# Kernel tuning notes

Measured on AMD Instinct MI355X. Metric: run time of the kernel, lower is better.

## Reference

```python
import jax, jax.numpy as jnp
import numpy as np

N, E, C, L, NG = 50000, 600000, 128, 7, 512
EPS = 1e-7


def layer_norm(z, g, b):
    mu = z.mean(-1, keepdims=True)
    var = ((z - mu) ** 2).mean(-1, keepdims=True)
    return (z - mu) * jax.lax.rsqrt(var + 1e-5) * g + b


def setup_inputs() -> dict:
    key = jax.random.key(0)
    ks = jax.random.split(key, 16)
    inp = {
        'x': jax.random.randint(ks[0], (N, 9), 0, 64, dtype=jnp.int32),
        'edge_index': jax.random.randint(ks[1], (2, E), 0, N, dtype=jnp.int32),
        'edge_attr': jax.random.randint(ks[2], (E, 3), 0, 8, dtype=jnp.int32),
        'batch': jnp.sort(jax.random.randint(ks[3], (N,), 0, NG, dtype=jnp.int32)),
        'atom_emb': jax.random.normal(ks[4], (9, 64, C), jnp.float32) * 0.1,
        'bond_emb': jax.random.normal(ks[5], (3, 8, C), jnp.float32) * 0.1,
        'vn_emb': jnp.zeros((1, C), jnp.float32),
        'conv_W1': jax.random.normal(ks[6], (L, C, 2 * C), jnp.float32) / np.sqrt(C),
        'conv_b1': jnp.zeros((L, 2 * C), jnp.float32),
        'conv_g1': jnp.ones((L, 2 * C), jnp.float32),
        'conv_bb1': jnp.zeros((L, 2 * C), jnp.float32),
        'conv_W2': jax.random.normal(ks[7], (L, 2 * C, C), jnp.float32) / np.sqrt(2 * C),
        'conv_b2': jnp.zeros((L, C), jnp.float32),
        'norm_g': jnp.ones((L, C), jnp.float32),
        'norm_b': jnp.zeros((L, C), jnp.float32),
        'vn_W1': jax.random.normal(ks[8], (L - 1, C, C), jnp.float32) / np.sqrt(C),
        'vn_b1': jnp.zeros((L - 1, C), jnp.float32),
        'vn_g': jnp.ones((L - 1, C), jnp.float32),
        'vn_bb': jnp.zeros((L - 1, C), jnp.float32),
        'vn_W2': jax.random.normal(ks[9], (L - 1, C, C), jnp.float32) / np.sqrt(C),
        'vn_b2': jnp.zeros((L - 1, C), jnp.float32),
    }
    return inp


def reference(x, edge_index, edge_attr, batch, atom_emb, bond_emb, vn_emb,
              conv_W1, conv_b1, conv_g1, conv_bb1, conv_W2, conv_b2,
              norm_g, norm_b, vn_W1, vn_b1, vn_g, vn_bb, vn_W2, vn_b2):
    src, dst = edge_index[0], edge_index[1]

    # AtomEncoder: sum of per-feature embeddings -> [N, C]
    h = atom_emb[jnp.arange(9), x].sum(axis=1)
    # BondEncoder (conv_encode_edge=False) -> [E, C]
    edge_emb = bond_emb[jnp.arange(3), edge_attr].sum(axis=1)

    # virtual node embedding (one per graph)
    vn = jnp.broadcast_to(vn_emb[0], (NG, C))
    h = h + vn[batch]

    def gen_conv(l, hx):
        # GENConv: msg = relu(x_j + e) + eps; softmax aggregation (t=1); MLP(x+m)
        msg = jax.nn.relu(hx[src] + edge_emb) + EPS                      # [E, C]
        mx = jax.ops.segment_max(msg, dst, num_segments=N)               # [N, C]
        e = jnp.exp(msg - mx[dst])
        den = jax.ops.segment_sum(e, dst, num_segments=N)
        m = jax.ops.segment_sum(msg * (e / (den[dst] + 1e-16)), dst, num_segments=N)
        z = hx + m
        z = jax.nn.relu(layer_norm(z @ conv_W1[l] + conv_b1[l], conv_g1[l], conv_bb1[l]))
        return z @ conv_W2[l] + conv_b2[l]

    # res+ block: Conv -> [Norm -> ReLU -> (VN update) -> Conv + res]*
    h = gen_conv(0, h)
    for l in range(1, L):
        h2 = jax.nn.relu(layer_norm(h, norm_g[l - 1], norm_b[l - 1]))
        vtmp = jax.ops.segment_sum(h2, batch, num_segments=NG) + vn
        v = jax.nn.relu(layer_norm(vtmp @ vn_W1[l - 1] + vn_b1[l - 1], vn_g[l - 1], vn_bb[l - 1]))
        vn = v @ vn_W2[l - 1] + vn_b2[l - 1]
        h2 = h2 + vn[batch]
        h = gen_conv(l, h2) + h
    h = layer_norm(h, norm_g[L - 1], norm_b[L - 1])

    # global_add_pool -> [NG, C]
    return jax.ops.segment_sum(h, batch, num_segments=NG)
```

## Files before the change

kernel.cpp:

```cpp
#include <hip/hip_runtime.h>
#include <hip/hip_bf16.h>
#include <stdint.h>

#define N_NODES 50000
#define N_EDGES 600000
#define CH 128
#define NLAYERS 7
#define NGRAPHS 512

typedef __hip_bfloat16 bf16;
using bf16x8 = __attribute__((ext_vector_type(8))) __bf16;
using f32x4  = __attribute__((ext_vector_type(4))) float;

static __device__ __forceinline__ float b2f(bf16 v){ return __bfloat162float(v); }

__global__ void k_detect(const uint32_t* __restrict__ g, int* __restrict__ flag){
  if (threadIdx.x == 0 && blockIdx.x == 0) flag[0] = (g[0] == 0x3F803F80u) ? 1 : 0;
}

struct Segs { const void* src[12]; float* dst[12]; int n[12]; };

__global__ void k_cvt_all(const int* __restrict__ flag, Segs S){
  int f = flag[0];
  int seg = blockIdx.y;
  int n = S.n[seg];
  const void* src = S.src[seg];
  float* dst = S.dst[seg];
  for (int i = blockIdx.x*blockDim.x + threadIdx.x; i < n; i += gridDim.x*blockDim.x)
    dst[i] = f ? b2f(((const bf16*)src)[i]) : ((const float*)src)[i];
}

__global__ void k_transpose_all(const int* __restrict__ flag,
    const void* W1, const void* W2, const void* vW1, const void* vW2,
    bf16* W1T, bf16* W2T, bf16* vW1T, bf16* vW2T){
  int f = flag[0];
  const int T0 = NLAYERS*128*256, T1 = NLAYERS*256*128;
  const int T2 = (NLAYERS-1)*128*128, T3 = (NLAYERS-1)*128*128;
  int total = T0+T1+T2+T3;
  for (int i = blockIdx.x*blockDim.x + threadIdx.x; i < total; i += gridDim.x*blockDim.x){
    const void* src; bf16* dst; int idx, R, C;
    if (i < T0){ src=W1; dst=W1T; idx=i; R=128; C=256; }
    else if (i < T0+T1){ src=W2; dst=W2T; idx=i-T0; R=256; C=128; }
    else if (i < T0+T1+T2){ src=vW1; dst=vW1T; idx=i-T0-T1; R=128; C=128; }
    else { src=vW2; dst=vW2T; idx=i-T0-T1-T2; R=128; C=128; }
    int l = idx/(R*C); int rem = idx - l*R*C; int r = rem / C; int c = rem - r*C;
    float v = f ? b2f(((const bf16*)src)[idx]) : ((const float*)src)[idx];
    dst[l*R*C + c*R + r] = __float2bfloat16(v);
  }
}

__global__ void k_bondC(const int* __restrict__ flag, const void* __restrict__ bond,
                        float* __restrict__ bondC){
  int f = flag[0];
  int i = blockIdx.x*blockDim.x + threadIdx.x;
  if (i >= 512*128) return;
  int idx = i >> 7, c = i & 127;
  int a0 = idx & 7, a1 = (idx>>3) & 7, a2 = (idx>>6) & 7;
  auto g = [&](int e)->float{ return f ? b2f(((const bf16*)bond)[e]) : ((const float*)bond)[e]; };
  bondC[i] = g((0*8+a0)*128 + c) + g((1*8+a1)*128 + c) + g((2*8+a2)*128 + c);
}

__global__ void k_zero_i32(int* p, int n){
  for (int i = blockIdx.x*blockDim.x + threadIdx.x; i < n; i += gridDim.x*blockDim.x) p[i] = 0;
}

__global__ void k_hist(const int* __restrict__ keys, int* __restrict__ counts, int n){
  for (int i = blockIdx.x*blockDim.x + threadIdx.x; i < n; i += gridDim.x*blockDim.x)
    atomicAdd(&counts[keys[i]], 1);
}

__global__ __launch_bounds__(256) void k_scanA(const int* __restrict__ in, int* __restrict__ out,
                                               int* __restrict__ bsums, int n){
  __shared__ int lds[256];
  int t = threadIdx.x;
  int base = blockIdx.x * 1024;
  int v[4]; int s = 0;
  #pragma unroll
  for (int i=0;i<4;i++){ int idx = base + t*4 + i; int x = (idx<n)? in[idx] : 0; v[i]=x; s+=x; }
  lds[t] = s; __syncthreads();
  for (int off=1; off<256; off<<=1){
    int x = (t>=off)? lds[t-off] : 0;
    __syncthreads();
    lds[t] += x;
    __syncthreads();
  }
  int p = lds[t] - s;
  #pragma unroll
  for (int i=0;i<4;i++){ int idx = base + t*4 + i; if (idx<n) out[idx] = p; p += v[i]; }
  if (t==255) bsums[blockIdx.x] = lds[255];
}

__global__ __launch_bounds__(256) void k_scanB(int* bsums, int nblk){
  __shared__ int lds[256];
  int t = threadIdx.x;
  int v = (t<nblk)? bsums[t] : 0;
  lds[t] = v; __syncthreads();
  for (int off=1; off<256; off<<=1){
    int x = (t>=off)? lds[t-off] : 0;
    __syncthreads();
    lds[t] += x;
    __syncthreads();
  }
  if (t<nblk) bsums[t] = lds[t] - v;
}

__global__ void k_scanC(int* out, const int* bsums, int n){
  for (int i = blockIdx.x*blockDim.x + threadIdx.x; i < n; i += gridDim.x*blockDim.x)
    out[i] += bsums[i >> 10];
}

__global__ void k_scatter(const int* __restrict__ ei, const int* __restrict__ ea,
                          const int* __restrict__ row_ptr, int* __restrict__ fill,
                          uint32_t* __restrict__ csr){
  for (int e = blockIdx.x*blockDim.x + threadIdx.x; e < N_EDGES; e += gridDim.x*blockDim.x){
    int src = ei[e];
    int dst = ei[N_EDGES + e];
    int pos = row_ptr[dst] + atomicAdd(&fill[dst], 1);
    uint32_t a0 = (uint32_t)ea[e*3+0], a1 = (uint32_t)ea[e*3+1], a2 = (uint32_t)ea[e*3+2];
    csr[pos] = (uint32_t)src | ((a0 | (a1<<3) | (a2<<6)) << 16);
  }
}

__global__ void k_gptr(const int* __restrict__ batch, int* __restrict__ gptr){
  int i = blockIdx.x*blockDim.x + threadIdx.x;
  if (i >= N_NODES) return;
  int b = batch[i];
  if (i == 0){ for (int g=0; g<=b; ++g) gptr[g] = 0; }
  else { int bp = batch[i-1]; for (int g=bp+1; g<=b; ++g) gptr[g] = i; }
  if (i == N_NODES-1){ for (int g=b+1; g<=NGRAPHS; ++g) gptr[g] = N_NODES; }
}

__global__ __launch_bounds__(128) void k_atom_encode(const int* __restrict__ x,
    const float* __restrict__ atom_emb, const float* __restrict__ vn_emb,
    uint32_t* __restrict__ hxb){
  int n = blockIdx.x; int c = threadIdx.x;
  float s = vn_emb[c];
  #pragma unroll
  for (int f=0; f<9; ++f){
    int xv = x[n*9+f];
    s += atom_emb[(f*64 + xv)*CH + c];
  }
  float o = __shfl_xor(s, 1);
  if ((c & 1) == 0){
    __hip_bfloat162 p; p.x = __float2bfloat16(s); p.y = __float2bfloat16(o);
    hxb[n*64 + (c>>1)] = *reinterpret_cast<uint32_t*>(&p);
  }
}

__global__ void k_vn_init(const float* __restrict__ vn_emb, float* __restrict__ vn){
  for (int i = blockIdx.x*blockDim.x + threadIdx.x; i < NGRAPHS*CH; i += gridDim.x*blockDim.x)
    vn[i] = vn_emb[i & (CH-1)];
}

__global__ __launch_bounds__(64) void k_aggregate(const uint32_t* __restrict__ hxb,
     const uint32_t* __restrict__ csr, const int* __restrict__ row_ptr,
     const float* __restrict__ bondC, uint32_t* __restrict__ z){
  int n = blockIdx.x; int t = threadIdx.x;
  int s0 = row_ptr[n], s1 = row_ptr[n+1];
  float sa=0.f, sb=0.f, wa=0.f, wb=0.f;
  int i = s0;
  for (; i+4 <= s1; i += 4){
    uint32_t u0=csr[i], u1=csr[i+1], u2=csr[i+2], u3=csr[i+3];
    uint32_t h0 = hxb[(size_t)(u0 & 0xFFFFu)*64 + t];
    uint32_t h1 = hxb[(size_t)(u1 & 0xFFFFu)*64 + t];
    uint32_t h2 = hxb[(size_t)(u2 & 0xFFFFu)*64 + t];
    uint32_t h3 = hxb[(size_t)(u3 & 0xFFFFu)*64 + t];
    float2 c0 = *reinterpret_cast<const float2*>(bondC + (size_t)(u0 >> 16)*128 + 2*t);
    float2 c1 = *reinterpret_cast<const float2*>(bondC + (size_t)(u1 >> 16)*128 + 2*t);
    float2 c2 = *reinterpret_cast<const float2*>(bondC + (size_t)(u2 >> 16)*128 + 2*t);
    float2 c3 = *reinterpret_cast<const float2*>(bondC + (size_t)(u3 >> 16)*128 + 2*t);
    #define EDGE(hp, bc) { \
      float va = __uint_as_float(hp << 16) + bc.x; \
      float vb = __uint_as_float(hp & 0xFFFF0000u) + bc.y; \
      va = fmaxf(va, 0.f) + 1e-7f; vb = fmaxf(vb, 0.f) + 1e-7f; \
      float pa = __expf(va - 10.f), pb = __expf(vb - 10.f); \
      sa += pa; wa += pa*va; sb += pb; wb += pb*vb; }
    EDGE(h0, c0) EDGE(h1, c1) EDGE(h2, c2) EDGE(h3, c3)
  }
  for (; i < s1; ++i){
    uint32_t u = csr[i];
    uint32_t hp = hxb[(size_t)(u & 0xFFFFu)*64 + t];
    float2 bc = *reinterpret_cast<const float2*>(bondC + (size_t)(u >> 16)*128 + 2*t);
    EDGE(hp, bc)
    #undef EDGE
  }
  uint32_t own = hxb[(size_t)n*64 + t];
  float za = __uint_as_float(own << 16)         + wa/(sa + 1e-16f);
  float zb = __uint_as_float(own & 0xFFFF0000u) + wb/(sb + 1e-16f);
  __hip_bfloat162 p; p.x = __float2bfloat16(za); p.y = __float2bfloat16(zb);
  z[(size_t)n*64 + t] = *reinterpret_cast<uint32_t*>(&p);
}

template<int K, int N1, int N2>
__global__ __launch_bounds__(512, 2) void k_mlp2(const bf16* __restrict__ A,
    const bf16* __restrict__ W1T, const float* __restrict__ b1,
    const float* __restrict__ g1, const float* __restrict__ bb1,
    const bf16* __restrict__ W2T, const float* __restrict__ b2,
    const float* __restrict__ residual, float* __restrict__ out, int M)
{
  constexpr int KK1 = K/32;
  constexpr int J1  = N1/16/8;
  constexpr int KK2 = N1/32;
  __shared__ float lnp[64][8][2];
  __shared__ float lnv[64][2];
  __shared__ __align__(16) bf16 zt[64*N1];
  const int tid = threadIdx.x;
  const int wid = tid >> 6, lane = tid & 63;
  const int rlo = lane & 15, hi = lane >> 4, khi = hi*8;
  const int row0 = blockIdx.x*64;

  bf16x8 B1[J1][KK1];
  #pragma unroll
  for (int jj=0;jj<J1;++jj){
    int col = (wid*J1 + jj)*16 + rlo;
    #pragma unroll
    for (int kk=0;kk<KK1;++kk)
      B1[jj][kk] = *reinterpret_cast<const bf16x8*>(W1T + (size_t)col*K + kk*32 + khi);
  }
  bf16x8 B2[KK2];
  #pragma unroll
  for (int kk=0;kk<KK2;++kk)
    B2[kk] = *reinterpret_cast<const bf16x8*>(W2T + (size_t)(wid*16 + rlo)*N1 + kk*32 + khi);

  f32x4 acc1[4][J1];
  #pragma unroll
  for (int t=0;t<4;++t)
    #pragma unroll
    for (int jj=0;jj<J1;++jj) acc1[t][jj] = {0.f,0.f,0.f,0.f};
  #pragma unroll
  for (int t=0;t<4;++t){
    int arow = row0 + t*16 + rlo; if (arow >= M) arow = M-1;
    const bf16* ap = A + (size_t)arow*K + khi;
    bf16x8 a[KK1];
    #pragma unroll
    for (int kk=0;kk<KK1;++kk) a[kk] = *reinterpret_cast<const bf16x8*>(ap + kk*32);
    #pragma unroll
    for (int kk=0;kk<KK1;++kk)
      #pragma unroll
      for (int jj=0;jj<J1;++jj)
        acc1[t][jj] = __builtin_amdgcn_mfma_f32_16x16x32_bf16(a[kk], B1[jj][kk], acc1[t][jj], 0,0,0);
  }

  float b1v[J1];
  #pragma unroll
  for (int jj=0;jj<J1;++jj) b1v[jj] = b1[(wid*J1+jj)*16 + rlo];
  float p[4][4], q[4][4];
  #pragma unroll
  for (int t=0;t<4;++t)
    #pragma unroll
    for (int r=0;r<4;++r){ p[t][r]=0.f; q[t][r]=0.f; }
  #pragma unroll
  for (int t=0;t<4;++t)
    #pragma unroll
    for (int jj=0;jj<J1;++jj)
      #pragma unroll
      for (int r=0;r<4;++r){
        float v = acc1[t][jj][r] + b1v[jj];
        acc1[t][jj][r] = v;
        p[t][r] += v; q[t][r] += v*v;
      }
  #pragma unroll
  for (int t=0;t<4;++t)
    #pragma unroll
    for (int r=0;r<4;++r){
      float pv = p[t][r], qv = q[t][r];
      #pragma unroll
      for (int off=1; off<16; off<<=1){ pv += __shfl_xor(pv, off); qv += __shfl_xor(qv, off); }
      if (rlo == 0){ int row = t*16 + hi*4 + r; lnp[row][wid][0] = pv; lnp[row][wid][1] = qv; }
    }
  __syncthreads();
  if (tid < 64){
    float P=0.f, Q=0.f;
    #pragma unroll
    for (int w=0;w<8;++w){ P += lnp[tid][w][0]; Q += lnp[tid][w][1]; }
    float mu = P*(1.f/N1);
    float var = Q*(1.f/N1) - mu*mu;
    lnv[tid][0] = mu; lnv[tid][1] = rsqrtf(var + 1e-5f);
  }
  __syncthreads();

  float gv[J1], bbv[J1];
  #pragma unroll
  for (int jj=0;jj<J1;++jj){ int col=(wid*J1+jj)*16+rlo; gv[jj]=g1[col]; bbv[jj]=bb1[col]; }
  #pragma unroll
  for (int t=0;t<4;++t)
    #pragma unroll
    for (int r=0;r<4;++r){
      int row = t*16 + hi*4 + r;
      float mu = lnv[row][0], rs = lnv[row][1];
      #pragma unroll
      for (int jj=0;jj<J1;++jj){
        int col = (wid*J1+jj)*16 + rlo;
        float y = (acc1[t][jj][r]-mu)*rs*gv[jj] + bbv[jj];
        y = fmaxf(y, 0.f);
        zt[(row*N1 + col) ^ ((row&7)<<3)] = __float2bfloat16(y);
      }
    }
  __syncthreads();

  f32x4 acc2[4];
  #pragma unroll
  for (int t=0;t<4;++t) acc2[t] = {0.f,0.f,0.f,0.f};
  #pragma unroll
  for (int t=0;t<4;++t){
    int row = t*16 + rlo;
    bf16x8 a2[KK2];
    #pragma unroll
    for (int kk=0;kk<KK2;++kk)
      a2[kk] = *reinterpret_cast<const bf16x8*>(&zt[(row*N1 + kk*32 + khi) ^ ((row&7)<<3)]);
    #pragma unroll
    for (int kk=0;kk<KK2;++kk)
      acc2[t] = __builtin_amdgcn_mfma_f32_16x16x32_bf16(a2[kk], B2[kk], acc2[t], 0,0,0);
  }

  float bv2 = b2[wid*16 + rlo];
  #pragma unroll
  for (int t=0;t<4;++t)
    #pragma unroll
    for (int r=0;r<4;++r){
      int grow = row0 + t*16 + hi*4 + r;
      if (grow < M){
        int col = wid*16 + rlo;
        float v = acc2[t][r] + bv2;
        if (residual) v += residual[(size_t)grow*N2 + col];
        out[(size_t)grow*N2 + col] = v;
      }
    }
}

__global__ __launch_bounds__(256) void k_ln_row(const float* __restrict__ in,
    const float* __restrict__ g, const float* __restrict__ b,
    float* __restrict__ outF, int rows, int relu)
{
  int wid = threadIdx.x >> 6, lane = threadIdx.x & 63;
  int row = blockIdx.x*4 + wid;
  if (row >= rows) return;
  const float* p = in + (size_t)row*CH;
  float x0 = p[lane], x1 = p[64+lane];
  float s = x0 + x1;
  #pragma unroll
  for (int off=32; off; off>>=1) s += __shfl_xor(s, off);
  float mu = s * (1.0f/CH);
  float d0 = x0-mu, d1 = x1-mu;
  float vs = d0*d0 + d1*d1;
  #pragma unroll
  for (int off=32; off; off>>=1) vs += __shfl_xor(vs, off);
  float rstd = rsqrtf(vs*(1.0f/CH) + 1e-5f);
  float y0 = d0*rstd*g[lane] + b[lane];
  float y1 = d1*rstd*g[64+lane] + b[64+lane];
  if (relu){ y0 = fmaxf(y0,0.f); y1 = fmaxf(y1,0.f); }
  outF[(size_t)row*CH + lane] = y0;
  outF[(size_t)row*CH + 64 + lane] = y1;
}

__global__ void k_vncopy(const float* __restrict__ vn, float* __restrict__ vnacc){
  int i = blockIdx.x*blockDim.x + threadIdx.x;
  if (i < NGRAPHS*CH) vnacc[i] = vn[i];
}

__global__ void k_prep_vtb(const float* __restrict__ vnacc, bf16* __restrict__ vtb){
  int i = blockIdx.x*blockDim.x + threadIdx.x;
  if (i < NGRAPHS*CH) vtb[i] = __float2bfloat16(vnacc[i]);
}

#define SEGC 128
__global__ __launch_bounds__(128) void k_segsum2(const float* __restrict__ hx,
    const int* __restrict__ batch, float* __restrict__ vnacc){
  int c = threadIdx.x;
  int n0 = blockIdx.x*SEGC;
  int n1 = n0 + SEGC; if (n1 > N_NODES) n1 = N_NODES;
  if (n0 >= N_NODES) return;
  int cur = batch[n0];
  float s = 0.f;
  for (int n = n0; n < n1; ++n){
    int b = batch[n];
    if (b != cur){ atomicAdd(&vnacc[cur*CH + c], s); s = 0.f; cur = b; }
    s += hx[(size_t)n*CH + c];
  }
  atomicAdd(&vnacc[cur*CH + c], s);
}

__global__ void k_add_vn(const float* __restrict__ hx, const float* __restrict__ vn,
                         const int* __restrict__ batch, uint32_t* __restrict__ hxb){
  for (int i = blockIdx.x*blockDim.x + threadIdx.x; i < N_NODES*64; i += gridDim.x*blockDim.x){
    int n = i >> 6; int t = i & 63;
    float2 hv = *reinterpret_cast<const float2*>(hx + (size_t)n*CH + 2*t);
    float2 vv = *reinterpret_cast<const float2*>(vn + (size_t)batch[n]*CH + 2*t);
    __hip_bfloat162 p; p.x = __float2bfloat16(hv.x+vv.x); p.y = __float2bfloat16(hv.y+vv.y);
    hxb[i] = *reinterpret_cast<uint32_t*>(&p);
  }
}

__global__ __launch_bounds__(128) void k_pool(const float* __restrict__ hx,
    const int* __restrict__ gptr, const int* __restrict__ flag, void* __restrict__ out){
  int g = blockIdx.x; int c = threadIdx.x;
  float s = 0.f;
  for (int n = gptr[g]; n < gptr[g+1]; ++n) s += hx[(size_t)n*CH + c];
  if (flag[0]) ((bf16*)out)[g*CH+c] = __float2bfloat16(s);
  else         ((float*)out)[g*CH+c] = s;
}

extern "C" void kernel_launch(void* const* d_in, const int* in_sizes, int n_in,
                              void* d_out, int out_size, void* d_ws, size_t ws_size,
                              hipStream_t stream)
{
  const int*  x     = (const int*) d_in[0];
  const int*  ei    = (const int*) d_in[1];
  const int*  ea    = (const int*) d_in[2];
  const int*  batch = (const int*) d_in[3];
  const void* atom_emb = d_in[4];
  const void* bond_emb = d_in[5];
  const void* vn_emb   = d_in[6];
  const void* conv_W1  = d_in[7];
  const void* conv_b1  = d_in[8];
  const void* conv_g1  = d_in[9];
  const void* conv_bb1 = d_in[10];
  const void* conv_W2  = d_in[11];
  const void* conv_b2  = d_in[12];
  const void* norm_g   = d_in[13];
  const void* norm_b   = d_in[14];
  const void* vn_W1    = d_in[15];
  const void* vn_b1    = d_in[16];
  const void* vn_g     = d_in[17];
  const void* vn_bb    = d_in[18];
  const void* vn_W2    = d_in[19];
  const void* vn_b2    = d_in[20];

  char* wsb = (char*)d_ws;
  size_t off = 0;
  auto alloc = [&](size_t bytes)->char*{ char* p = wsb + off; off += (bytes + 255) & ~(size_t)255; return p; };
  float*    h     = (float*)   alloc(sizeof(float)*N_NODES*CH);
  float*    hx    = (float*)   alloc(sizeof(float)*N_NODES*CH);
  uint32_t* hxb   = (uint32_t*)alloc(sizeof(uint32_t)*N_NODES*64);
  uint32_t* z     = (uint32_t*)alloc(sizeof(uint32_t)*N_NODES*64);
  float*    vn    = (float*)   alloc(sizeof(float)*NGRAPHS*CH);
  float*    vnacc = (float*)   alloc(sizeof(float)*NGRAPHS*CH);
  bf16*     vtb   = (bf16*)    alloc(sizeof(bf16)*NGRAPHS*CH);
  bf16*     W1T   = (bf16*)    alloc(sizeof(bf16)*NLAYERS*CH*2*CH);
  bf16*     W2T   = (bf16*)    alloc(sizeof(bf16)*NLAYERS*2*CH*CH);
  bf16*     vW1T  = (bf16*)    alloc(sizeof(bf16)*(NLAYERS-1)*CH*CH);
  bf16*     vW2T  = (bf16*)    alloc(sizeof(bf16)*(NLAYERS-1)*CH*CH);
  int* row_ptr = (int*)alloc(sizeof(int)*(N_NODES+1));
  int* counts  = (int*)alloc(sizeof(int)*(N_NODES+1));
  uint32_t* csr = (uint32_t*)alloc(sizeof(uint32_t)*N_EDGES);
  int* gptr    = (int*)alloc(sizeof(int)*(NGRAPHS+1));
  int* bsums   = (int*)alloc(sizeof(int)*256);
  int* flag    = (int*)alloc(sizeof(int)*64);
  float* atomF = (float*)alloc(sizeof(float)*9*64*CH);
  float* bondC = (float*)alloc(sizeof(float)*512*CH);
  float* vnEF  = (float*)alloc(sizeof(float)*CH);
  float* b1F   = (float*)alloc(sizeof(float)*NLAYERS*2*CH);
  float* g1F   = (float*)alloc(sizeof(float)*NLAYERS*2*CH);
  float* bb1F  = (float*)alloc(sizeof(float)*NLAYERS*2*CH);
  float* b2F   = (float*)alloc(sizeof(float)*NLAYERS*CH);
  float* ngF   = (float*)alloc(sizeof(float)*NLAYERS*CH);
  float* nbF   = (float*)alloc(sizeof(float)*NLAYERS*CH);
  float* vb1F  = (float*)alloc(sizeof(float)*(NLAYERS-1)*CH);
  float* vgF   = (float*)alloc(sizeof(float)*(NLAYERS-1)*CH);
  float* vbbF  = (float*)alloc(sizeof(float)*(NLAYERS-1)*CH);
  float* vb2F  = (float*)alloc(sizeof(float)*(NLAYERS-1)*CH);

  k_detect<<<1, 64, 0, stream>>>((const uint32_t*)norm_g, flag);
  Segs S;
  int si = 0;
  auto seg = [&](const void* s_, float* d_, int n_){ S.src[si]=s_; S.dst[si]=d_; S.n[si]=n_; ++si; };
  seg(atom_emb, atomF, 9*64*CH);
  seg(vn_emb,   vnEF,  CH);
  seg(conv_b1,  b1F,  NLAYERS*2*CH);
  seg(conv_g1,  g1F,  NLAYERS*2*CH);
  seg(conv_bb1, bb1F, NLAYERS*2*CH);
  seg(conv_b2,  b2F,  NLAYERS*CH);
  seg(norm_g,   ngF,  NLAYERS*CH);
  seg(norm_b,   nbF,  NLAYERS*CH);
  seg(vn_b1,    vb1F, (NLAYERS-1)*CH);
  seg(vn_g,     vgF,  (NLAYERS-1)*CH);
  seg(vn_bb,    vbbF, (NLAYERS-1)*CH);
  seg(vn_b2,    vb2F, (NLAYERS-1)*CH);
  k_cvt_all<<<dim3(72, 12), 256, 0, stream>>>(flag, S);
  k_transpose_all<<<640, 256, 0, stream>>>(flag, conv_W1, conv_W2, vn_W1, vn_W2,
                                           W1T, W2T, vW1T, vW2T);
  k_bondC<<<256, 256, 0, stream>>>(flag, bond_emb, bondC);

  k_zero_i32<<<64, 256, 0, stream>>>(counts, N_NODES+1);
  k_hist<<<512, 256, 0, stream>>>(ei + N_EDGES, counts, N_EDGES);
  int nblkE = (N_NODES+1 + 1023)/1024;
  k_scanA<<<nblkE, 256, 0, stream>>>(counts, row_ptr, bsums, N_NODES+1);
  k_scanB<<<1, 256, 0, stream>>>(bsums, nblkE);
  k_scanC<<<64, 256, 0, stream>>>(row_ptr, bsums, N_NODES+1);
  k_zero_i32<<<64, 256, 0, stream>>>(counts, N_NODES+1);
  k_scatter<<<512, 256, 0, stream>>>(ei, ea, row_ptr, counts, csr);
  k_gptr<<<(N_NODES+255)/256, 256, 0, stream>>>(batch, gptr);

  k_atom_encode<<<N_NODES, 128, 0, stream>>>(x, atomF, vnEF, hxb);
  k_vn_init<<<64, 256, 0, stream>>>(vnEF, vn);

  int mlpBlocks = (N_NODES + 63)/64;
  int lnBlocksN = (N_NODES + 3)/4;

  for (int l = 0; l < NLAYERS; ++l){
    if (l > 0){
      k_ln_row<<<lnBlocksN, 256, 0, stream>>>(h, ngF + (l-1)*CH, nbF + (l-1)*CH, hx, N_NODES, 1);
      k_vncopy<<<(NGRAPHS*CH+255)/256, 256, 0, stream>>>(vn, vnacc);
      k_segsum2<<<(N_NODES+SEGC-1)/SEGC, 128, 0, stream>>>(hx, batch, vnacc);
      k_prep_vtb<<<(NGRAPHS*CH+255)/256, 256, 0, stream>>>(vnacc, vtb);
      k_mlp2<128,128,128><<<NGRAPHS/64, 512, 0, stream>>>(vtb,
          vW1T + (size_t)(l-1)*CH*CH, vb1F + (l-1)*CH, vgF + (l-1)*CH, vbbF + (l-1)*CH,
          vW2T + (size_t)(l-1)*CH*CH, vb2F + (l-1)*CH, nullptr, vn, NGRAPHS);
      k_add_vn<<<1024, 256, 0, stream>>>(hx, vn, batch, hxb);
    }
    k_aggregate<<<N_NODES, 64, 0, stream>>>(hxb, csr, row_ptr, bondC, z);
    k_mlp2<128,256,128><<<mlpBlocks, 512, 0, stream>>>((const bf16*)z,
        W1T + (size_t)l*CH*2*CH, b1F + l*2*CH, g1F + l*2*CH, bb1F + l*2*CH,
        W2T + (size_t)l*2*CH*CH, b2F + l*CH, (l==0)? nullptr : h, h, N_NODES);
  }
  k_ln_row<<<lnBlocksN, 256, 0, stream>>>(h, ngF + (NLAYERS-1)*CH, nbF + (NLAYERS-1)*CH,
                                          hx, N_NODES, 0);
  k_pool<<<NGRAPHS, 128, 0, stream>>>(hx, gptr, flag, d_out);
}
```

Measured before the change: 1.174 ms.

## Stage swizzled W1 in LDS via direct loads and give each wave its own rows

The fused two-GEMM MLP kernel is restructured. Each block now handles 128 rows, and each wave owns 16 full rows instead of a column slice. W1 is pre-swizzled at transpose time and copied into LDS with global_load_lds, and the LayerNorm row statistics are reduced entirely within a wave, so the cross-wave LDS reduction and one barrier go away. The aim is less redundant per-wave W1 register loading and less synchronization. In exchange the kernel uses more LDS, reuses that buffer for the intermediate, and launches half as many blocks.

```diff
diff --git a/kernel.cpp b/kernel.cpp
--- a/kernel.cpp
+++ b/kernel.cpp
@@ -38,14 +38,15 @@
   const int T2 = (NLAYERS-1)*128*128, T3 = (NLAYERS-1)*128*128;
   int total = T0+T1+T2+T3;
   for (int i = blockIdx.x*blockDim.x + threadIdx.x; i < total; i += gridDim.x*blockDim.x){
-    const void* src; bf16* dst; int idx, R, C;
-    if (i < T0){ src=W1; dst=W1T; idx=i; R=128; C=256; }
-    else if (i < T0+T1){ src=W2; dst=W2T; idx=i-T0; R=256; C=128; }
-    else if (i < T0+T1+T2){ src=vW1; dst=vW1T; idx=i-T0-T1; R=128; C=128; }
-    else { src=vW2; dst=vW2T; idx=i-T0-T1-T2; R=128; C=128; }
+    const void* src; bf16* dst; int idx, R, C, swz;
+    if (i < T0){ src=W1; dst=W1T; idx=i; R=128; C=256; swz=1; }
+    else if (i < T0+T1){ src=W2; dst=W2T; idx=i-T0; R=256; C=128; swz=0; }
+    else if (i < T0+T1+T2){ src=vW1; dst=vW1T; idx=i-T0-T1; R=128; C=128; swz=1; }
+    else { src=vW2; dst=vW2T; idx=i-T0-T1-T2; R=128; C=128; swz=0; }
     int l = idx/(R*C); int rem = idx - l*R*C; int r = rem / C; int c = rem - r*C;
     float v = f ? b2f(((const bf16*)src)[idx]) : ((const float*)src)[idx];
-    dst[l*R*C + c*R + r] = __float2bfloat16(v);
+    int rr = swz ? (r ^ ((c&7)<<3)) : r;
+    dst[l*R*C + c*R + rr] = __float2bfloat16(v);
   }
 }
 
@@ -192,140 +193,126 @@
 }
 
 template<int K, int N1, int N2>
-__global__ __launch_bounds__(512, 2) void k_mlp2(const bf16* __restrict__ A,
-    const bf16* __restrict__ W1T, const float* __restrict__ b1,
+__global__ __launch_bounds__(512, 2) void k_mlp3(const bf16* __restrict__ A,
+    const bf16* __restrict__ W1s, const float* __restrict__ b1,
     const float* __restrict__ g1, const float* __restrict__ bb1,
     const bf16* __restrict__ W2T, const float* __restrict__ b2,
     const float* __restrict__ residual, float* __restrict__ out, int M)
 {
   constexpr int KK1 = K/32;
-  constexpr int J1  = N1/16/8;
+  constexpr int NJ1 = N1/16;
   constexpr int KK2 = N1/32;
-  __shared__ float lnp[64][8][2];
-  __shared__ float lnv[64][2];
-  __shared__ __align__(16) bf16 zt[64*N1];
+  constexpr int BM  = 128;
+  constexpr int W1E = K*N1;
+  constexpr int ZTE = BM*N1;
+  constexpr int SME = (W1E > ZTE) ? W1E : ZTE;
+  __shared__ __align__(16) bf16 smem[SME];
+
   const int tid = threadIdx.x;
   const int wid = tid >> 6, lane = tid & 63;
   const int rlo = lane & 15, hi = lane >> 4, khi = hi*8;
-  const int row0 = blockIdx.x*64;
-
-  bf16x8 B1[J1][KK1];
-  #pragma unroll
-  for (int jj=0;jj<J1;++jj){
-    int col = (wid*J1 + jj)*16 + rlo;
-    #pragma unroll
-    for (int kk=0;kk<KK1;++kk)
-      B1[jj][kk] = *reinterpret_cast<const bf16x8*>(W1T + (size_t)col*K + kk*32 + khi);
-  }
+  const int row0 = blockIdx.x*BM;
+
+  constexpr int PASSES = (W1E*2) / 8192;
+  {
+    const char* g = (const char*)W1s;
+    char* l = (char*)&smem[0];
+    #pragma unroll
+    for (int p=0;p<PASSES;++p){
+      int off = p*8192 + wid*1024;
+      __builtin_amdgcn_global_load_lds((const uint32_t*)(g + off + lane*16),
+                                       (uint32_t*)(l + off), 16, 0, 0);
+    }
+  }
+  int arow = row0 + wid*16 + rlo; if (arow >= M) arow = M-1;
+  bf16x8 a[KK1];
+  #pragma unroll
+  for (int kk=0;kk<KK1;++kk)
+    a[kk] = *reinterpret_cast<const bf16x8*>(A + (size_t)arow*K + kk*32 + khi);
+  __syncthreads();
+
+  f32x4 acc1[NJ1];
+  #pragma unroll
+  for (int j=0;j<NJ1;++j) acc1[j] = {0.f,0.f,0.f,0.f};
+  #pragma unroll
+  for (int j=0;j<NJ1;++j){
+    int col = j*16 + rlo;
+    int cs  = (col&7)<<3;
+    #pragma unroll
+    for (int kk=0;kk<KK1;++kk){
+      bf16x8 b = *reinterpret_cast<const bf16x8*>(&smem[col*K + ((kk*32 + khi) ^ cs)]);
+      acc1[j] = __builtin_amdgcn_mfma_f32_16x16x32_bf16(a[kk], b, acc1[j], 0, 0, 0);
+    }
+  }
+
+  float p[4] = {0,0,0,0}, q[4] = {0,0,0,0};
+  #pragma unroll
+  for (int j=0;j<NJ1;++j){
+    float bv = b1[j*16 + rlo];
+    #pragma unroll
+    for (int r=0;r<4;++r){
+      float v = acc1[j][r] + bv; acc1[j][r] = v;
+      p[r] += v; q[r] += v*v;
+    }
+  }
+  #pragma unroll
+  for (int r=0;r<4;++r){
+    #pragma unroll
+    for (int off=1; off<16; off<<=1){
+      p[r] += __shfl_xor(p[r], off);
+      q[r] += __shfl_xor(q[r], off);
+    }
+  }
+  float mu[4], rs[4];
+  #pragma unroll
+  for (int r=0;r<4;++r){
+    mu[r] = p[r]*(1.f/N1);
+    rs[r] = rsqrtf(q[r]*(1.f/N1) - mu[r]*mu[r] + 1e-5f);
+  }
+
+  __syncthreads();
+  #pragma unroll
+  for (int j=0;j<NJ1;++j){
+    int col = j*16 + rlo;
+    float gv = g1[col], bbv = bb1[col];
+    #pragma unroll
+    for (int r=0;r<4;++r){
+      int row = wid*16 + hi*4 + r;
+      float y = (acc1[j][r]-mu[r])*rs[r]*gv + bbv;
+      y = fmaxf(y, 0.f);
+      smem[row*N1 + (col ^ ((row&7)<<3))] = __float2bfloat16(y);
+    }
+  }
+  __syncthreads();
+
   bf16x8 B2[KK2];
   #pragma unroll
   for (int kk=0;kk<KK2;++kk)
     B2[kk] = *reinterpret_cast<const bf16x8*>(W2T + (size_t)(wid*16 + rlo)*N1 + kk*32 + khi);
-
-  f32x4 acc1[4][J1];
-  #pragma unroll
-  for (int t=0;t<4;++t)
-    #pragma unroll
-    for (int jj=0;jj<J1;++jj) acc1[t][jj] = {0.f,0.f,0.f,0.f};
-  #pragma unroll
-  for (int t=0;t<4;++t){
-    int arow = row0 + t*16 + rlo; if (arow >= M) arow = M-1;
-    const bf16* ap = A + (size_t)arow*K + khi;
-    bf16x8 a[KK1];
-    #pragma unroll
-    for (int kk=0;kk<KK1;++kk) a[kk] = *reinterpret_cast<const bf16x8*>(ap + kk*32);
-    #pragma unroll
-    for (int kk=0;kk<KK1;++kk)
-      #pragma unroll
-      for (int jj=0;jj<J1;++jj)
-        acc1[t][jj] = __builtin_amdgcn_mfma_f32_16x16x32_bf16(a[kk], B1[jj][kk], acc1[t][jj], 0,0,0);
-  }
-
-  float b1v[J1];
-  #pragma unroll
-  for (int jj=0;jj<J1;++jj) b1v[jj] = b1[(wid*J1+jj)*16 + rlo];
-  float p[4][4], q[4][4];
-  #pragma unroll
-  for (int t=0;t<4;++t)
-    #pragma unroll
-    for (int r=0;r<4;++r){ p[t][r]=0.f; q[t][r]=0.f; }
-  #pragma unroll
-  for (int t=0;t<4;++t)
-    #pragma unroll
-    for (int jj=0;jj<J1;++jj)
-      #pragma unroll
-      for (int r=0;r<4;++r){
-        float v = acc1[t][jj][r] + b1v[jj];
-        acc1[t][jj][r] = v;
-        p[t][r] += v; q[t][r] += v*v;
-      }
-  #pragma unroll
-  for (int t=0;t<4;++t)
-    #pragma unroll
-    for (int r=0;r<4;++r){
-      float pv = p[t][r], qv = q[t][r];
-      #pragma unroll
-      for (int off=1; off<16; off<<=1){ pv += __shfl_xor(pv, off); qv += __shfl_xor(qv, off); }
-      if (rlo == 0){ int row = t*16 + hi*4 + r; lnp[row][wid][0] = pv; lnp[row][wid][1] = qv; }
-    }
-  __syncthreads();
-  if (tid < 64){
-    float P=0.f, Q=0.f;
-    #pragma unroll
-    for (int w=0;w<8;++w){ P += lnp[tid][w][0]; Q += lnp[tid][w][1]; }
-    float mu = P*(1.f/N1);
-    float var = Q*(1.f/N1) - mu*mu;
-    lnv[tid][0] = mu; lnv[tid][1] = rsqrtf(var + 1e-5f);
-  }
-  __syncthreads();
-
-  float gv[J1], bbv[J1];
-  #pragma unroll
-  for (int jj=0;jj<J1;++jj){ int col=(wid*J1+jj)*16+rlo; gv[jj]=g1[col]; bbv[jj]=bb1[col]; }
-  #pragma unroll
-  for (int t=0;t<4;++t)
-    #pragma unroll
-    for (int r=0;r<4;++r){
-      int row = t*16 + hi*4 + r;
-      float mu = lnv[row][0], rs = lnv[row][1];
-      #pragma unroll
-      for (int jj=0;jj<J1;++jj){
-        int col = (wid*J1+jj)*16 + rlo;
-        float y = (acc1[t][jj][r]-mu)*rs*gv[jj] + bbv[jj];
-        y = fmaxf(y, 0.f);
-        zt[(row*N1 + col) ^ ((row&7)<<3)] = __float2bfloat16(y);
-      }
-    }
-  __syncthreads();
-
-  f32x4 acc2[4];
-  #pragma unroll
-  for (int t=0;t<4;++t) acc2[t] = {0.f,0.f,0.f,0.f};
-  #pragma unroll
-  for (int t=0;t<4;++t){
-    int row = t*16 + rlo;
+  float bv2 = b2[wid*16 + rlo];
+  #pragma unroll
+  for (int t=0;t<BM/16;++t){
+    int zrow = t*16 + rlo;
+    int zs = (zrow&7)<<3;
     bf16x8 a2[KK2];
     #pragma unroll
     for (int kk=0;kk<KK2;++kk)
-      a2[kk] = *reinterpret_cast<const bf16x8*>(&zt[(row*N1 + kk*32 + khi) ^ ((row&7)<<3)]);
+      a2[kk] = *reinterpret_cast<const bf16x8*>(&smem[zrow*N1 + ((kk*32 + khi) ^ zs)]);
+    f32x4 acc2 = {0.f,0.f,0.f,0.f};
     #pragma unroll
     for (int kk=0;kk<KK2;++kk)
-      acc2[t] = __builtin_amdgcn_mfma_f32_16x16x32_bf16(a2[kk], B2[kk], acc2[t], 0,0,0);
-  }
-
-  float bv2 = b2[wid*16 + rlo];
-  #pragma unroll
-  for (int t=0;t<4;++t)
+      acc2 = __builtin_amdgcn_mfma_f32_16x16x32_bf16(a2[kk], B2[kk], acc2, 0, 0, 0);
     #pragma unroll
     for (int r=0;r<4;++r){
       int grow = row0 + t*16 + hi*4 + r;
       if (grow < M){
         int col = wid*16 + rlo;
-        float v = acc2[t][r] + bv2;
+        float v = acc2[r] + bv2;
         if (residual) v += residual[(size_t)grow*N2 + col];
         out[(size_t)grow*N2 + col] = v;
       }
     }
+  }
 }
 
 __global__ __launch_bounds__(256) void k_ln_row(const float* __restrict__ in,
@@ -494,7 +481,7 @@
   k_atom_encode<<<N_NODES, 128, 0, stream>>>(x, atomF, vnEF, hxb);
   k_vn_init<<<64, 256, 0, stream>>>(vnEF, vn);
 
-  int mlpBlocks = (N_NODES + 63)/64;
+  int mlpBlocks = (N_NODES + 127)/128;
   int lnBlocksN = (N_NODES + 3)/4;
 
   for (int l = 0; l < NLAYERS; ++l){
@@ -503,13 +490,13 @@
       k_vncopy<<<(NGRAPHS*CH+255)/256, 256, 0, stream>>>(vn, vnacc);
       k_segsum2<<<(N_NODES+SEGC-1)/SEGC, 128, 0, stream>>>(hx, batch, vnacc);
       k_prep_vtb<<<(NGRAPHS*CH+255)/256, 256, 0, stream>>>(vnacc, vtb);
-      k_mlp2<128,128,128><<<NGRAPHS/64, 512, 0, stream>>>(vtb,
+      k_mlp3<128,128,128><<<NGRAPHS/128, 512, 0, stream>>>(vtb,
           vW1T + (size_t)(l-1)*CH*CH, vb1F + (l-1)*CH, vgF + (l-1)*CH, vbbF + (l-1)*CH,
           vW2T + (size_t)(l-1)*CH*CH, vb2F + (l-1)*CH, nullptr, vn, NGRAPHS);
       k_add_vn<<<1024, 256, 0, stream>>>(hx, vn, batch, hxb);
     }
     k_aggregate<<<N_NODES, 64, 0, stream>>>(hxb, csr, row_ptr, bondC, z);
-    k_mlp2<128,256,128><<<mlpBlocks, 512, 0, stream>>>((const bf16*)z,
+    k_mlp3<128,256,128><<<mlpBlocks, 512, 0, stream>>>((const bf16*)z,
         W1T + (size_t)l*CH*2*CH, b1F + l*2*CH, g1F + l*2*CH, bb1F + l*2*CH,
         W2T + (size_t)l*2*CH*CH, b2F + l*CH, (l==0)? nullptr : h, h, N_NODES);
   }
```

Result: faster. 1.110 ms (-5.4%).

## Make fused MLP persistent with LDS-resident W1 and double-buffered A tiles

Applied to the files above, without the earlier changes.

Replaces the one-tile-per-block fused MLP kernel with a persistent kernel (256 blocks looping over 64-row tiles). Each block loads W1 once into LDS with padded rows (K+8) and prefetches the next A tile into a second LDS buffer via global_load_lds while it computes the current tile. Warps use a 2x4 row/column split instead of column-only. The z buffer and the weight/vtb layouts are padded to 136/68-element rows so these are direct LDS copies without bank conflicts. Risks: the large LDS footprint limits occupancy, and the vn MLP gains little because it has only 8 tiles.

```diff
diff --git a/kernel.cpp b/kernel.cpp
--- a/kernel.cpp
+++ b/kernel.cpp
@@ -32,20 +32,33 @@
 
 __global__ void k_transpose_all(const int* __restrict__ flag,
     const void* W1, const void* W2, const void* vW1, const void* vW2,
-    bf16* W1T, bf16* W2T, bf16* vW1T, bf16* vW2T){
+    bf16* W1p, bf16* W2T, bf16* vW1p, bf16* vW2T){
   int f = flag[0];
   const int T0 = NLAYERS*128*256, T1 = NLAYERS*256*128;
   const int T2 = (NLAYERS-1)*128*128, T3 = (NLAYERS-1)*128*128;
   int total = T0+T1+T2+T3;
   for (int i = blockIdx.x*blockDim.x + threadIdx.x; i < total; i += gridDim.x*blockDim.x){
-    const void* src; bf16* dst; int idx, R, C;
-    if (i < T0){ src=W1; dst=W1T; idx=i; R=128; C=256; }
-    else if (i < T0+T1){ src=W2; dst=W2T; idx=i-T0; R=256; C=128; }
-    else if (i < T0+T1+T2){ src=vW1; dst=vW1T; idx=i-T0-T1; R=128; C=128; }
-    else { src=vW2; dst=vW2T; idx=i-T0-T1-T2; R=128; C=128; }
-    int l = idx/(R*C); int rem = idx - l*R*C; int r = rem / C; int c = rem - r*C;
-    float v = f ? b2f(((const bf16*)src)[idx]) : ((const float*)src)[idx];
-    dst[l*R*C + c*R + r] = __float2bfloat16(v);
+    float v; int didx;
+    if (i < T0){
+      int idx = i; int l = idx/(128*256); int rem = idx - l*128*256; int k = rem >> 8; int n = rem & 255;
+      v = f ? b2f(((const bf16*)W1)[idx]) : ((const float*)W1)[idx];
+      W1p[(size_t)l*256*136 + n*136 + k] = __float2bfloat16(v);
+      continue;
+    } else if (i < T0+T1){
+      int idx = i-T0; int l = idx/(256*128); int rem = idx - l*256*128; int k = rem >> 7; int n = rem & 127;
+      v = f ? b2f(((const bf16*)W2)[idx]) : ((const float*)W2)[idx];
+      W2T[(size_t)l*128*256 + n*256 + k] = __float2bfloat16(v);
+      continue;
+    } else if (i < T0+T1+T2){
+      int idx = i-T0-T1; int l = idx/(128*128); int rem = idx - l*128*128; int k = rem >> 7; int n = rem & 127;
+      v = f ? b2f(((const bf16*)vW1)[idx]) : ((const float*)vW1)[idx];
+      vW1p[(size_t)l*128*136 + n*136 + k] = __float2bfloat16(v);
+      continue;
+    } else {
+      int idx = i-T0-T1-T2; int l = idx/(128*128); int rem = idx - l*128*128; int k = rem >> 7; int n = rem & 127;
+      v = f ? b2f(((const bf16*)vW2)[idx]) : ((const float*)vW2)[idx];
+      vW2T[(size_t)l*128*128 + n*128 + k] = __float2bfloat16(v);
+    }
   }
 }
 
@@ -188,144 +201,185 @@
   float za = __uint_as_float(own << 16)         + wa/(sa + 1e-16f);
   float zb = __uint_as_float(own & 0xFFFF0000u) + wb/(sb + 1e-16f);
   __hip_bfloat162 p; p.x = __float2bfloat16(za); p.y = __float2bfloat16(zb);
-  z[(size_t)n*64 + t] = *reinterpret_cast<uint32_t*>(&p);
+  z[(size_t)n*68 + t] = *reinterpret_cast<uint32_t*>(&p);
 }
 
 template<int K, int N1, int N2>
-__global__ __launch_bounds__(512, 2) void k_mlp2(const bf16* __restrict__ A,
-    const bf16* __restrict__ W1T, const float* __restrict__ b1,
-    const float* __restrict__ g1, const float* __restrict__ bb1,
-    const bf16* __restrict__ W2T, const float* __restrict__ b2,
-    const float* __restrict__ residual, float* __restrict__ out, int M)
+__global__ __launch_bounds__(512, 2) void k_mlp5(const bf16* __restrict__ A,
+    const bf16* __restrict__ W1p,
+    const float* __restrict__ b1, const float* __restrict__ g1, const float* __restrict__ bb1,
+    const bf16* __restrict__ W2T,
+    const float* __restrict__ b2,
+    const float* __restrict__ residual, float* __restrict__ out, int M, int NT)
 {
+  constexpr int KP  = K + 8;
   constexpr int KK1 = K/32;
-  constexpr int J1  = N1/16/8;
+  constexpr int WC  = N1/4;
+  constexpr int JC  = WC/16;
   constexpr int KK2 = N1/32;
-  __shared__ float lnp[64][8][2];
-  __shared__ float lnv[64][2];
-  __shared__ __align__(16) bf16 zt[64*N1];
+  constexpr int ZTP = N1 + 8;
+  constexpr int W1B = N1*KP*2;
+  constexpr int AB  = 64*KP*2;
+  constexpr int W1CH = W1B/1024;
+  constexpr int ACH  = AB/1024;
+
+  __shared__ __align__(16) char smem[W1B + 2*AB + 64*ZTP*2 + 64*4*2*4 + 64*2*4];
+  bf16* W1L = (bf16*)smem;
+  bf16* Ab0 = (bf16*)(smem + W1B);
+  bf16* Ab1 = (bf16*)(smem + W1B + AB);
+  bf16* zt  = (bf16*)(smem + W1B + 2*AB);
+  float* lnp = (float*)(smem + W1B + 2*AB + 64*ZTP*2);
+  float* lnv = (float*)(smem + W1B + 2*AB + 64*ZTP*2 + 2048);
+
   const int tid = threadIdx.x;
   const int wid = tid >> 6, lane = tid & 63;
+  const int wr = wid >> 2, wc = wid & 3;
   const int rlo = lane & 15, hi = lane >> 4, khi = hi*8;
-  const int row0 = blockIdx.x*64;
-
-  bf16x8 B1[J1][KK1];
-  #pragma unroll
-  for (int jj=0;jj<J1;++jj){
-    int col = (wid*J1 + jj)*16 + rlo;
-    #pragma unroll
-    for (int kk=0;kk<KK1;++kk)
-      B1[jj][kk] = *reinterpret_cast<const bf16x8*>(W1T + (size_t)col*K + kk*32 + khi);
-  }
-  bf16x8 B2[KK2];
-  #pragma unroll
-  for (int kk=0;kk<KK2;++kk)
-    B2[kk] = *reinterpret_cast<const bf16x8*>(W2T + (size_t)(wid*16 + rlo)*N1 + kk*32 + khi);
-
-  f32x4 acc1[4][J1];
-  #pragma unroll
-  for (int t=0;t<4;++t)
-    #pragma unroll
-    for (int jj=0;jj<J1;++jj) acc1[t][jj] = {0.f,0.f,0.f,0.f};
-  #pragma unroll
-  for (int t=0;t<4;++t){
-    int arow = row0 + t*16 + rlo; if (arow >= M) arow = M-1;
-    const bf16* ap = A + (size_t)arow*K + khi;
-    bf16x8 a[KK1];
-    #pragma unroll
-    for (int kk=0;kk<KK1;++kk) a[kk] = *reinterpret_cast<const bf16x8*>(ap + kk*32);
-    #pragma unroll
-    for (int kk=0;kk<KK1;++kk)
-      #pragma unroll
-      for (int jj=0;jj<J1;++jj)
-        acc1[t][jj] = __builtin_amdgcn_mfma_f32_16x16x32_bf16(a[kk], B1[jj][kk], acc1[t][jj], 0,0,0);
-  }
-
-  float b1v[J1];
-  #pragma unroll
-  for (int jj=0;jj<J1;++jj) b1v[jj] = b1[(wid*J1+jj)*16 + rlo];
-  float p[4][4], q[4][4];
-  #pragma unroll
-  for (int t=0;t<4;++t)
-    #pragma unroll
-    for (int r=0;r<4;++r){ p[t][r]=0.f; q[t][r]=0.f; }
-  #pragma unroll
-  for (int t=0;t<4;++t)
-    #pragma unroll
-    for (int jj=0;jj<J1;++jj)
+
+  for (int c = wid; c < W1CH; c += 8)
+    __builtin_amdgcn_global_load_lds((const uint32_t*)((const char*)W1p + c*1024 + lane*16),
+                                     (uint32_t*)((char*)W1L + c*1024), 16, 0, 0);
+
+  auto stageA = [&](bf16* dst, int tile){
+    const char* src = (const char*)A + (size_t)tile*AB;
+    for (int c = wid; c < ACH; c += 8)
+      __builtin_amdgcn_global_load_lds((const uint32_t*)(src + c*1024 + lane*16),
+                                       (uint32_t*)((char*)dst + c*1024), 16, 0, 0);
+  };
+
+  int t = blockIdx.x;
+  stageA(Ab0, t);
+  __syncthreads();
+  int cur = 0;
+
+  while (true){
+    int tn = t + (int)gridDim.x;
+    const bf16* Ac = cur ? Ab1 : Ab0;
+
+    f32x4 acc1[2][JC];
+    #pragma unroll
+    for (int rt=0;rt<2;++rt)
+      #pragma unroll
+      for (int jc=0;jc<JC;++jc) acc1[rt][jc] = {0.f,0.f,0.f,0.f};
+    #pragma unroll
+    for (int kk=0;kk<KK1;++kk){
+      bf16x8 af[2], bf_[JC];
+      #pragma unroll
+      for (int rt=0;rt<2;++rt)
+        af[rt] = *reinterpret_cast<const bf16x8*>(Ac + (wr*32 + rt*16 + rlo)*KP + kk*32 + khi);
+      #pragma unroll
+      for (int jc=0;jc<JC;++jc)
+        bf_[jc] = *reinterpret_cast<const bf16x8*>(W1L + (wc*WC + jc*16 + rlo)*KP + kk*32 + khi);
+      #pragma unroll
+      for (int rt=0;rt<2;++rt)
+        #pragma unroll
+        for (int jc=0;jc<JC;++jc)
+          acc1[rt][jc] = __builtin_amdgcn_mfma_f32_16x16x32_bf16(af[rt], bf_[jc], acc1[rt][jc], 0,0,0);
+    }
+
+    float p[2][4], q[2][4];
+    #pragma unroll
+    for (int rt=0;rt<2;++rt)
+      #pragma unroll
+      for (int r=0;r<4;++r){ p[rt][r]=0.f; q[rt][r]=0.f; }
+    #pragma unroll
+    for (int jc=0;jc<JC;++jc){
+      float bv = b1[wc*WC + jc*16 + rlo];
+      #pragma unroll
+      for (int rt=0;rt<2;++rt)
+        #pragma unroll
+        for (int r=0;r<4;++r){
+          float v = acc1[rt][jc][r] + bv; acc1[rt][jc][r] = v;
+          p[rt][r] += v; q[rt][r] += v*v;
+        }
+    }
+    #pragma unroll
+    for (int rt=0;rt<2;++rt)
       #pragma unroll
       for (int r=0;r<4;++r){
-        float v = acc1[t][jj][r] + b1v[jj];
-        acc1[t][jj][r] = v;
-        p[t][r] += v; q[t][r] += v*v;
+        float pv = p[rt][r], qv = q[rt][r];
+        #pragma unroll
+        for (int off=1; off<16; off<<=1){ pv += __shfl_xor(pv, off); qv += __shfl_xor(qv, off); }
+        if (rlo == 0){
+          int row = wr*32 + rt*16 + hi*4 + r;
+          lnp[(row*4 + wc)*2 + 0] = pv;
+          lnp[(row*4 + wc)*2 + 1] = qv;
+        }
       }
-  #pragma unroll
-  for (int t=0;t<4;++t)
-    #pragma unroll
-    for (int r=0;r<4;++r){
-      float pv = p[t][r], qv = q[t][r];
-      #pragma unroll
-      for (int off=1; off<16; off<<=1){ pv += __shfl_xor(pv, off); qv += __shfl_xor(qv, off); }
-      if (rlo == 0){ int row = t*16 + hi*4 + r; lnp[row][wid][0] = pv; lnp[row][wid][1] = qv; }
-    }
-  __syncthreads();
-  if (tid < 64){
-    float P=0.f, Q=0.f;
-    #pragma unroll
-    for (int w=0;w<8;++w){ P += lnp[tid][w][0]; Q += lnp[tid][w][1]; }
-    float mu = P*(1.f/N1);
-    float var = Q*(1.f/N1) - mu*mu;
-    lnv[tid][0] = mu; lnv[tid][1] = rsqrtf(var + 1e-5f);
-  }
-  __syncthreads();
-
-  float gv[J1], bbv[J1];
-  #pragma unroll
-  for (int jj=0;jj<J1;++jj){ int col=(wid*J1+jj)*16+rlo; gv[jj]=g1[col]; bbv[jj]=bb1[col]; }
-  #pragma unroll
-  for (int t=0;t<4;++t)
-    #pragma unroll
-    for (int r=0;r<4;++r){
-      int row = t*16 + hi*4 + r;
-      float mu = lnv[row][0], rs = lnv[row][1];
-      #pragma unroll
-      for (int jj=0;jj<J1;++jj){
-        int col = (wid*J1+jj)*16 + rlo;
-        float y = (acc1[t][jj][r]-mu)*rs*gv[jj] + bbv[jj];
-        y = fmaxf(y, 0.f);
-        zt[(row*N1 + col) ^ ((row&7)<<3)] = __float2bfloat16(y);
+    __syncthreads();
+    if (tid < 64){
+      float P=0.f, Q=0.f;
+      #pragma unroll
+      for (int w=0;w<4;++w){ P += lnp[(tid*4+w)*2]; Q += lnp[(tid*4+w)*2+1]; }
+      float mu = P*(1.f/N1);
+      lnv[tid*2]   = mu;
+      lnv[tid*2+1] = rsqrtf(Q*(1.f/N1) - mu*mu + 1e-5f);
+    }
+    __syncthreads();
+
+    #pragma unroll
+    for (int rt=0;rt<2;++rt)
+      #pragma unroll
+      for (int r=0;r<4;++r){
+        int row = wr*32 + rt*16 + hi*4 + r;
+        float mu = lnv[row*2], rs = lnv[row*2+1];
+        #pragma unroll
+        for (int jc=0;jc<JC;++jc){
+          int col = wc*WC + jc*16 + rlo;
+          float y = (acc1[rt][jc][r]-mu)*rs*g1[col] + bb1[col];
+          zt[row*ZTP + col] = __float2bfloat16(fmaxf(y, 0.f));
+        }
       }
-    }
-  __syncthreads();
-
-  f32x4 acc2[4];
-  #pragma unroll
-  for (int t=0;t<4;++t) acc2[t] = {0.f,0.f,0.f,0.f};
-  #pragma unroll
-  for (int t=0;t<4;++t){
-    int row = t*16 + rlo;
-    bf16x8 a2[KK2];
-    #pragma unroll
-    for (int kk=0;kk<KK2;++kk)
-      a2[kk] = *reinterpret_cast<const bf16x8*>(&zt[(row*N1 + kk*32 + khi) ^ ((row&7)<<3)]);
-    #pragma unroll
-    for (int kk=0;kk<KK2;++kk)
-      acc2[t] = __builtin_amdgcn_mfma_f32_16x16x32_bf16(a2[kk], B2[kk], acc2[t], 0,0,0);
-  }
-
-  float bv2 = b2[wid*16 + rlo];
-  #pragma unroll
-  for (int t=0;t<4;++t)
-    #pragma unroll
-    for (int r=0;r<4;++r){
-      int grow = row0 + t*16 + hi*4 + r;
-      if (grow < M){
-        int col = wid*16 + rlo;
-        float v = acc2[t][r] + bv2;
-        if (residual) v += residual[(size_t)grow*N2 + col];
-        out[(size_t)grow*N2 + col] = v;
-      }
-    }
+    __syncthreads();
+
+    if (tn < NT) stageA(cur ? Ab0 : Ab1, tn);
+
+    bf16x8 B2f[2][KK2];
+    #pragma unroll
+    for (int ct=0;ct<2;++ct){
+      const bf16* wp = W2T + (size_t)(wc*32 + ct*16 + rlo)*N1 + khi;
+      #pragma unroll
+      for (int kk=0;kk<KK2;++kk)
+        B2f[ct][kk] = *reinterpret_cast<const bf16x8*>(wp + kk*32);
+    }
+    f32x4 acc2[2][2];
+    #pragma unroll
+    for (int rt=0;rt<2;++rt)
+      #pragma unroll
+      for (int ct=0;ct<2;++ct) acc2[rt][ct] = {0.f,0.f,0.f,0.f};
+    #pragma unroll
+    for (int kk=0;kk<KK2;++kk){
+      bf16x8 a2[2];
+      #pragma unroll
+      for (int rt=0;rt<2;++rt)
+        a2[rt] = *reinterpret_cast<const bf16x8*>(zt + (wr*32 + rt*16 + rlo)*ZTP + kk*32 + khi);
+      #pragma unroll
+      for (int rt=0;rt<2;++rt)
+        #pragma unroll
+        for (int ct=0;ct<2;++ct)
+          acc2[rt][ct] = __builtin_amdgcn_mfma_f32_16x16x32_bf16(a2[rt], B2f[ct][kk], acc2[rt][ct], 0,0,0);
+    }
+    #pragma unroll
+    for (int ct=0;ct<2;++ct){
+      int col = wc*32 + ct*16 + rlo;
+      float bv = b2[col];
+      #pragma unroll
+      for (int rt=0;rt<2;++rt)
+        #pragma unroll
+        for (int r=0;r<4;++r){
+          int grow = t*64 + wr*32 + rt*16 + hi*4 + r;
+          if (grow < M){
+            float v = acc2[rt][ct][r] + bv;
+            if (residual) v += residual[(size_t)grow*N2 + col];
+            out[(size_t)grow*N2 + col] = v;
+          }
+        }
+    }
+
+    if (tn >= NT) break;
+    __syncthreads();
+    t = tn; cur ^= 1;
+  }
 }
 
 __global__ __launch_bounds__(256) void k_ln_row(const float* __restrict__ in,
@@ -360,7 +414,7 @@
 
 __global__ void k_prep_vtb(const float* __restrict__ vnacc, bf16* __restrict__ vtb){
   int i = blockIdx.x*blockDim.x + threadIdx.x;
-  if (i < NGRAPHS*CH) vtb[i] = __float2bfloat16(vnacc[i]);
+  if (i < NGRAPHS*CH) vtb[(i>>7)*136 + (i&127)] = __float2bfloat16(vnacc[i]);
 }
 
 #define SEGC 128
@@ -429,17 +483,18 @@
   char* wsb = (char*)d_ws;
   size_t off = 0;
   auto alloc = [&](size_t bytes)->char*{ char* p = wsb + off; off += (bytes + 255) & ~(size_t)255; return p; };
+  const int ZROWS = 50048;
   float*    h     = (float*)   alloc(sizeof(float)*N_NODES*CH);
   float*    hx    = (float*)   alloc(sizeof(float)*N_NODES*CH);
   uint32_t* hxb   = (uint32_t*)alloc(sizeof(uint32_t)*N_NODES*64);
-  uint32_t* z     = (uint32_t*)alloc(sizeof(uint32_t)*N_NODES*64);
+  uint32_t* z     = (uint32_t*)alloc(sizeof(uint32_t)*ZROWS*68);
   float*    vn    = (float*)   alloc(sizeof(float)*NGRAPHS*CH);
   float*    vnacc = (float*)   alloc(sizeof(float)*NGRAPHS*CH);
-  bf16*     vtb   = (bf16*)    alloc(sizeof(bf16)*NGRAPHS*CH);
-  bf16*     W1T   = (bf16*)    alloc(sizeof(bf16)*NLAYERS*CH*2*CH);
-  bf16*     W2T   = (bf16*)    alloc(sizeof(bf16)*NLAYERS*2*CH*CH);
-  bf16*     vW1T  = (bf16*)    alloc(sizeof(bf16)*(NLAYERS-1)*CH*CH);
-  bf16*     vW2T  = (bf16*)    alloc(sizeof(bf16)*(NLAYERS-1)*CH*CH);
+  bf16*     vtb   = (bf16*)    alloc(sizeof(bf16)*NGRAPHS*136);
+  bf16*     W1Tp  = (bf16*)    alloc(sizeof(bf16)*NLAYERS*256*136);
+  bf16*     W2T   = (bf16*)    alloc(sizeof(bf16)*NLAYERS*128*256);
+  bf16*     vW1Tp = (bf16*)    alloc(sizeof(bf16)*(NLAYERS-1)*128*136);
+  bf16*     vW2T  = (bf16*)    alloc(sizeof(bf16)*(NLAYERS-1)*128*128);
   int* row_ptr = (int*)alloc(sizeof(int)*(N_NODES+1));
   int* counts  = (int*)alloc(sizeof(int)*(N_NODES+1));
   uint32_t* csr = (uint32_t*)alloc(sizeof(uint32_t)*N_EDGES);
@@ -478,7 +533,7 @@
   seg(vn_b2,    vb2F, (NLAYERS-1)*CH);
   k_cvt_all<<<dim3(72, 12), 256, 0, stream>>>(flag, S);
   k_transpose_all<<<640, 256, 0, stream>>>(flag, conv_W1, conv_W2, vn_W1, vn_W2,
-                                           W1T, W2T, vW1T, vW2T);
+                                           W1Tp, W2T, vW1Tp, vW2T);
   k_bondC<<<256, 256, 0, stream>>>(flag, bond_emb, bondC);
 
   k_zero_i32<<<64, 256, 0, stream>>>(counts, N_NODES+1);
@@ -494,8 +549,9 @@
   k_atom_encode<<<N_NODES, 128, 0, stream>>>(x, atomF, vnEF, hxb);
   k_vn_init<<<64, 256, 0, stream>>>(vnEF, vn);
 
-  int mlpBlocks = (N_NODES + 63)/64;
   int lnBlocksN = (N_NODES + 3)/4;
+  const int NT_CONV = (N_NODES + 63)/64;
+  const int NT_VN   = NGRAPHS/64;
 
   for (int l = 0; l < NLAYERS; ++l){
     if (l > 0){
@@ -503,15 +559,15 @@
       k_vncopy<<<(NGRAPHS*CH+255)/256, 256, 0, stream>>>(vn, vnacc);
       k_segsum2<<<(N_NODES+SEGC-1)/SEGC, 128, 0, stream>>>(hx, batch, vnacc);
       k_prep_vtb<<<(NGRAPHS*CH+255)/256, 256, 0, stream>>>(vnacc, vtb);
-      k_mlp2<128,128,128><<<NGRAPHS/64, 512, 0, stream>>>(vtb,
-          vW1T + (size_t)(l-1)*CH*CH, vb1F + (l-1)*CH, vgF + (l-1)*CH, vbbF + (l-1)*CH,
-          vW2T + (size_t)(l-1)*CH*CH, vb2F + (l-1)*CH, nullptr, vn, NGRAPHS);
+      k_mlp5<128,128,128><<<NT_VN, 512, 0, stream>>>(vtb,
+          vW1Tp + (size_t)(l-1)*128*136, vb1F + (l-1)*CH, vgF + (l-1)*CH, vbbF + (l-1)*CH,
+          vW2T + (size_t)(l-1)*128*128, vb2F + (l-1)*CH, nullptr, vn, NGRAPHS, NT_VN);
       k_add_vn<<<1024, 256, 0, stream>>>(hx, vn, batch, hxb);
     }
     k_aggregate<<<N_NODES, 64, 0, stream>>>(hxb, csr, row_ptr, bondC, z);
-    k_mlp2<128,256,128><<<mlpBlocks, 512, 0, stream>>>((const bf16*)z,
-        W1T + (size_t)l*CH*2*CH, b1F + l*2*CH, g1F + l*2*CH, bb1F + l*2*CH,
-        W2T + (size_t)l*2*CH*CH, b2F + l*CH, (l==0)? nullptr : h, h, N_NODES);
+    k_mlp5<128,256,128><<<256, 512, 0, stream>>>((const bf16*)z,
+        W1Tp + (size_t)l*256*136, b1F + l*2*CH, g1F + l*2*CH, bb1F + l*2*CH,
+        W2T + (size_t)l*128*256, b2F + l*CH, (l==0)? nullptr : h, h, N_NODES, NT_CONV);
   }
   k_ln_row<<<lnBlocksN, 256, 0, stream>>>(h, ngF + (NLAYERS-1)*CH, nbF + (NLAYERS-1)*CH,
                                           hx, N_NODES, 0);
```

Measured after the change: 1.045 ms. 11.0% less time.
